# Kernel tuning notes

Measured on AMD Instinct MI355X. Metric: run time of the kernel, lower is better.

The kernel has to match this reference:

```python
import jax, jax.numpy as jnp
import numpy as np

B, T, D = 2, 2048, 2048
HK, HV, K, V = 16, 32, 128, 128          # key heads, value heads, head dims
KEY_DIM, VALUE_DIM = HK * K, HV * V      # 2048, 4096
CONV_W = 4                               # causal conv kernel width
EPS = 1e-6


def setup_inputs() -> dict:
    key = jax.random.key(0)
    ks = jax.random.split(key, 8)
    rn = lambda k, shp, sc: jax.random.normal(k, shp, dtype=jnp.float32) * sc
    return {
        "hidden_states": rn(ks[0], (B, T, D), 1.0),
        "W_qkvz": rn(ks[1], (D, 2 * KEY_DIM + 2 * VALUE_DIM), D ** -0.5),
        "W_ba": rn(ks[2], (D, 2 * HV), D ** -0.5),
        "conv_weight": rn(ks[3], (2 * KEY_DIM + VALUE_DIM, CONV_W), CONV_W ** -0.5),
        "A_log": jnp.log(jax.random.uniform(ks[4], (HV,), minval=1.0, maxval=16.0)),
        "dt_bias": rn(ks[5], (HV,), 0.5),
        "norm_weight": jnp.zeros((V,), jnp.float32),  # zero-centered RMSNorm weight
        "W_out": rn(ks[6], (VALUE_DIM, D), VALUE_DIM ** -0.5),
    }


def _l2norm(x):
    return x * jax.lax.rsqrt(jnp.sum(x * x, axis=-1, keepdims=True) + 1e-6)


def _causal_conv_silu(x, w):
    # x: [B,T,C]; depthwise causal conv, kernel width CONV_W, then SiLU
    xp = jnp.pad(x, ((0, 0), (CONV_W - 1, 0), (0, 0)))
    out = sum(xp[:, j:j + x.shape[1], :] * w[None, None, :, j] for j in range(CONV_W))
    return jax.nn.silu(out)


def _gated_delta_rule(q, k, v, g, beta):
    # q,k: [B,T,HV,K] (l2-normed, q pre-scaled); v: [B,T,HV,V]; g,beta: [B,T,HV]
    def step(S, xs):                      # S: [B,HV,K,V]
        q_t, k_t, v_t, g_t, beta_t = xs
        S = S * jnp.exp(g_t)[..., None, None]
        pred = jnp.einsum('bhk,bhkv->bhv', k_t, S)
        delta = (v_t - pred) * beta_t[..., None]
        S = S + jnp.einsum('bhk,bhv->bhkv', k_t, delta)
        o_t = jnp.einsum('bhk,bhkv->bhv', q_t, S)
        return S, o_t

    mv = lambda x: jnp.moveaxis(x, 1, 0)  # time-major for scan
    S0 = jnp.zeros((q.shape[0], HV, K, V), q.dtype)
    _, o = jax.lax.scan(step, S0, (mv(q), mv(k), mv(v), mv(g), mv(beta)))
    return jnp.moveaxis(o, 0, 1)          # [B,T,HV,V]


def reference(hidden_states, W_qkvz, W_ba, conv_weight, A_log, dt_bias,
              norm_weight, W_out):
    b_, t_ = hidden_states.shape[:2]
    qkvz = hidden_states @ W_qkvz
    q, k, v, z = jnp.split(qkvz, [KEY_DIM, 2 * KEY_DIM, 2 * KEY_DIM + VALUE_DIM], axis=-1)
    ba = hidden_states @ W_ba
    b_gate, a = jnp.split(ba, 2, axis=-1)  # each [B,T,HV]

    # fused causal conv1d + SiLU over concat(q,k,v)
    mixed = _causal_conv_silu(jnp.concatenate([q, k, v], axis=-1), conv_weight)
    q, k, v = jnp.split(mixed, [KEY_DIM, 2 * KEY_DIM], axis=-1)

    # gating: beta = sigmoid(b), g = -exp(A_log) * softplus(a + dt_bias)
    beta = jax.nn.sigmoid(b_gate)
    g = -jnp.exp(A_log) * jax.nn.softplus(a + dt_bias)

    # GQA expand (v_per_k_group = HV // HK), l2norm, scale
    rep = HV // HK
    q = jnp.repeat(q.reshape(b_, t_, HK, K), rep, axis=2)
    k = jnp.repeat(k.reshape(b_, t_, HK, K), rep, axis=2)
    v = v.reshape(b_, t_, HV, V)
    q = _l2norm(q) * (K ** -0.5)
    k = _l2norm(k)

    o = _gated_delta_rule(q, k, v, g, beta)  # [B,T,HV,V]

    # gated RMSNorm (per value head, zero-centered weight) then out projection
    zg = z.reshape(b_, t_, HV, V)
    x = o * jax.nn.silu(zg)
    var = jnp.mean(x * x, axis=-1, keepdims=True)
    x = x * jax.lax.rsqrt(var + EPS) * (1.0 + norm_weight)
    return x.reshape(b_, t_, VALUE_DIM) @ W_out
```

## Files before the change

kernel.cpp:

```cpp
#include <hip/hip_runtime.h>

typedef unsigned short u16;
typedef unsigned int u32;

typedef short bf16x8 __attribute__((ext_vector_type(8)));
typedef float f32x4 __attribute__((ext_vector_type(4)));
typedef float f32x16 __attribute__((ext_vector_type(16)));

#define T_SEQ 2048
#define MFMA16(a, b, c) __builtin_amdgcn_mfma_f32_16x16x32_bf16(a, b, c, 0, 0, 0)
#define MFMA32(a, b, c) __builtin_amdgcn_mfma_f32_32x32x16_bf16(a, b, c, 0, 0, 0)

__device__ __forceinline__ u16 f2bf(float f) {
    u32 u = __float_as_uint(f);
    u += 0x7fffu + ((u >> 16) & 1u);
    return (u16)(u >> 16);
}
__device__ __forceinline__ float bf2f(u16 s) {
    return __uint_as_float(((u32)s) << 16);
}
__device__ __forceinline__ void g2lds16(const u16* gp, u16* lp) {
    __builtin_amdgcn_global_load_lds((const __attribute__((address_space(1))) void*)gp,
                                     (__attribute__((address_space(3))) void*)lp, 16, 0, 0);
}

__global__ __launch_bounds__(256) void cast_f32_bf16(const float* __restrict__ in,
                                                     u16* __restrict__ out, long n) {
    long i = ((long)blockIdx.x * 256 + threadIdx.x) * 4;
    if (i + 3 < n) {
        float4 v = *(const float4*)&in[i];
        out[i + 0] = f2bf(v.x);
        out[i + 1] = f2bf(v.y);
        out[i + 2] = f2bf(v.z);
        out[i + 3] = f2bf(v.w);
    }
}

__global__ __launch_bounds__(256) void transpose_cast(const float* __restrict__ in,
                                                      u16* __restrict__ out, int R, int C) {
    __shared__ float tile[32][33];
    int c0 = blockIdx.x * 32, r0 = blockIdx.y * 32;
    int tx = threadIdx.x & 31, ty = threadIdx.x >> 5;
#pragma unroll
    for (int rr = 0; rr < 32; rr += 8)
        tile[ty + rr][tx] = in[(long)(r0 + ty + rr) * C + c0 + tx];
    __syncthreads();
#pragma unroll
    for (int rr = 0; rr < 32; rr += 8)
        out[(long)(c0 + ty + rr) * R + r0 + tx] = f2bf(tile[tx][ty + rr]);
}

template <int MODE>
__global__ __launch_bounds__(256) void gemm_bt(const u16* __restrict__ A,
                                               const u16* __restrict__ B, void* __restrict__ C,
                                               void* __restrict__ C2, int M, int N, int K, int lda,
                                               int ldb, int ldc) {
    __shared__ __align__(16) u16 As[128 * 64];
    __shared__ __align__(16) u16 Bs[128 * 64];
    int m0 = blockIdx.x * 128, n0 = blockIdx.y * 128;
    int tid = threadIdx.x;
    int lane = tid & 63, w = tid >> 6;
    int wr = w >> 1, wc = w & 1;
    int l31 = lane & 31, hf = lane >> 5;

    f32x16 acc[2][2];
#pragma unroll
    for (int mi = 0; mi < 2; mi++)
#pragma unroll
        for (int nj = 0; nj < 2; nj++)
#pragma unroll
            for (int r = 0; r < 16; r++) acc[mi][nj][r] = 0.f;

    int srow = tid >> 3;
    int sc8 = ((tid & 7) ^ ((tid >> 3) & 7)) * 8;
    const u16* Ag = &A[(long)(m0 + srow) * lda + sc8];
    const u16* Bg = &B[(long)(n0 + srow) * ldb + sc8];

    for (int k0 = 0; k0 < K; k0 += 64) {
#pragma unroll
        for (int p = 0; p < 4; p++) {
            g2lds16(Ag + (long)p * 32 * lda + k0, &As[(p * 256 + tid) * 8]);
            g2lds16(Bg + (long)p * 32 * ldb + k0, &Bs[(p * 256 + tid) * 8]);
        }
        __syncthreads();
#pragma unroll
        for (int ks = 0; ks < 4; ks++) {
            int cell = ((ks * 2 + hf) ^ (l31 & 7)) * 8;
            bf16x8 a0 = *(const bf16x8*)&As[(wr * 64 + l31) * 64 + cell];
            bf16x8 a1 = *(const bf16x8*)&As[(wr * 64 + 32 + l31) * 64 + cell];
            bf16x8 b0 = *(const bf16x8*)&Bs[(wc * 64 + l31) * 64 + cell];
            bf16x8 b1 = *(const bf16x8*)&Bs[(wc * 64 + 32 + l31) * 64 + cell];
            acc[0][0] = MFMA32(a0, b0, acc[0][0]);
            acc[0][1] = MFMA32(a0, b1, acc[0][1]);
            acc[1][0] = MFMA32(a1, b0, acc[1][0]);
            acc[1][1] = MFMA32(a1, b1, acc[1][1]);
        }
        __syncthreads();
    }

    if (MODE == 0) {
#pragma unroll
        for (int mi = 0; mi < 2; mi++)
#pragma unroll
            for (int nj = 0; nj < 2; nj++)
#pragma unroll
                for (int r = 0; r < 16; r++) {
                    int row = m0 + wr * 64 + mi * 32 + (r >> 2) * 8 + hf * 4 + (r & 3);
                    int col = n0 + wc * 64 + nj * 32 + l31;
                    ((float*)C)[(long)row * ldc + col] = acc[mi][nj][r];
                }
    } else {
        u16* dst;
        long dldc;
        int ncol0;
        if (MODE == 2 && n0 >= 8192) {
            dst = (u16*)C2;
            dldc = 4096;
            ncol0 = n0 - 8192;
        } else {
            dst = (u16*)C;
            dldc = (MODE == 2) ? 8192 : ldc;
            ncol0 = n0;
        }
#pragma unroll 1
        for (int half_e = 0; half_e < 2; half_e++) {
            __syncthreads();
            if (wc == half_e) {
#pragma unroll
                for (int mi = 0; mi < 2; mi++)
#pragma unroll
                    for (int nj = 0; nj < 2; nj++)
#pragma unroll
                        for (int r = 0; r < 16; r++) {
                            int row = wr * 64 + mi * 32 + (r >> 2) * 8 + hf * 4 + (r & 3);
                            int col = nj * 32 + l31;
                            u16* base = (row < 64) ? As : Bs;
                            base[(row & 63) * 64 + col] = f2bf(acc[mi][nj][r]);
                        }
            }
            __syncthreads();
#pragma unroll
            for (int rr = 0; rr < 4; rr++) {
                int row = rr * 32 + (tid >> 3), seg = tid & 7;
                u16* base = (row < 64) ? As : Bs;
                *(uint4*)&dst[(long)(m0 + row) * dldc + ncol0 + half_e * 64 + seg * 8] =
                    *(uint4*)&base[(row & 63) * 64 + seg * 8];
            }
        }
    }
}

#define VM8 asm volatile("s_waitcnt vmcnt(8)" ::: "memory")
#define VM4 asm volatile("s_waitcnt vmcnt(4)" ::: "memory")
#define VM0 asm volatile("s_waitcnt vmcnt(0)" ::: "memory")
#define VMNONE ((void)0)

#define STAGE_A(S, R2)                       \
    do {                                     \
        u16* Ld = &sbuf[(R2) * 16384];       \
        long ko = (long)(S) * 32;            \
        g2lds16(pA0 + ko, Ld + dA0);         \
        g2lds16(pA1 + ko, Ld + dA1);         \
    } while (0)
#define STAGE_B(S, R2)                          \
    do {                                        \
        u16* Ld = &sbuf[(R2) * 16384 + 8192];   \
        long ko = (long)(S) * 32;               \
        g2lds16(pB0 + ko, Ld + dA0);            \
        g2lds16(pB1 + ko, Ld + dA1);            \
    } while (0)

#define MQUAD(RB, AV)                          \
    acc[RB][0] = MFMA16(AV, b0, acc[RB][0]);   \
    acc[RB][1] = MFMA16(AV, b1, acc[RB][1]);   \
    acc[RB][2] = MFMA16(AV, b2, acc[RB][2]);   \
    acc[RB][3] = MFMA16(AV, b3, acc[RB][3]);

#define GITER(RING, S3, STG, VMSTMT)                                        \
    {                                                                       \
        const u16* LA = &sbuf[(RING) * 16384 + wm8 * 512 + lane8];          \
        const u16* LB = &sbuf[(RING) * 16384 + 8192 + wn4 * 512 + lane8];   \
        bf16x8 b0 = *(const bf16x8*)&LB[0];                                 \
        bf16x8 b1 = *(const bf16x8*)&LB[512];                               \
        bf16x8 b2 = *(const bf16x8*)&LB[1024];                              \
        bf16x8 b3 = *(const bf16x8*)&LB[1536];                              \
        bf16x8 a0 = *(const bf16x8*)&LA[0];                                 \
        bf16x8 a1 = *(const bf16x8*)&LA[512];                               \
        bf16x8 a2 = *(const bf16x8*)&LA[1024];                              \
        bf16x8 a3 = *(const bf16x8*)&LA[1536];                              \
        bf16x8 a4 = *(const bf16x8*)&LA[2048];                              \
        bf16x8 a5 = *(const bf16x8*)&LA[2560];                              \
        bf16x8 a6 = *(const bf16x8*)&LA[3072];                              \
        bf16x8 a7 = *(const bf16x8*)&LA[3584];                              \
        if (STG) {                                                          \
            STAGE_A(S3, ((RING) + 3) & 3);                                  \
            STAGE_B(S3, ((RING) + 3) & 3);                                  \
        }                                                                   \
        __builtin_amdgcn_s_setprio(1);                                      \
        MQUAD(0, a0)                                                        \
        MQUAD(1, a1)                                                        \
        MQUAD(2, a2)                                                        \
        MQUAD(3, a3)                                                        \
        MQUAD(4, a4)                                                        \
        MQUAD(5, a5)                                                        \
        MQUAD(6, a6)                                                        \
        MQUAD(7, a7)                                                        \
        __builtin_amdgcn_s_setprio(0);                                      \
        VMSTMT;                                                             \
        __builtin_amdgcn_s_barrier();                                       \
        __builtin_amdgcn_sched_barrier(0);                                  \
    }

__global__ __launch_bounds__(512, 2) void gemm256(const u16* __restrict__ A,
                                                  const u16* __restrict__ B,
                                                  u16* __restrict__ Cq, u16* __restrict__ Cz) {
    __shared__ __align__(16) u16 sbuf[65536];
    int bid = blockIdx.x;
    int swz = (bid & 7) * 96 + (bid >> 3);
    int m0 = (swz & 15) * 256;
    int n0 = (swz >> 4) * 256;
    int tid = threadIdx.x;
    int lane = tid & 63, w = tid >> 6;
    int l15 = lane & 15, quad = lane >> 4;
    int wm8 = (w >> 2) * 8, wn4 = (w & 3) * 4;
    int lane8 = lane * 8;
    int dA0 = w * 512 + lane8, dA1 = w * 512 + lane8 + 4096;
    const u16* pA0 = &A[(long)(m0 + w * 16 + l15) * 2048 + quad * 8];
    const u16* pA1 = pA0 + 128L * 2048;
    const u16* pB0 = &B[(long)(n0 + w * 16 + l15) * 2048 + quad * 8];
    const u16* pB1 = pB0 + 128L * 2048;

    f32x4 acc[8][4];
#pragma unroll
    for (int i = 0; i < 8; i++)
#pragma unroll
        for (int j = 0; j < 4; j++) acc[i][j] = (f32x4){0.f, 0.f, 0.f, 0.f};

    STAGE_A(0, 0);
    STAGE_B(0, 0);
    STAGE_A(1, 1);
    STAGE_B(1, 1);
    STAGE_A(2, 2);
    STAGE_B(2, 2);
    VM8;
    __builtin_amdgcn_s_barrier();
    __builtin_amdgcn_sched_barrier(0);

    for (int it = 0; it < 60; it += 4) {
        GITER(0, it + 3, 1, VM8);
        GITER(1, it + 4, 1, VM8);
        GITER(2, it + 5, 1, VM8);
        GITER(3, it + 6, 1, VM8);
    }
    GITER(0, 63, 1, VM8);
    GITER(1, 0, 0, VM4);
    GITER(2, 0, 0, VM0);
    GITER(3, 0, 0, VMNONE);

#pragma unroll
    for (int rb = 0; rb < 8; rb++)
#pragma unroll
        for (int cb = 0; cb < 4; cb++)
#pragma unroll
            for (int r = 0; r < 4; r++) {
                int row = wm8 * 16 + rb * 16 + quad * 4 + r;
                int col = wn4 * 16 + cb * 16 + l15;
                int cg = col >> 4;
                int phys = row * 256 + ((cg ^ (row & 7)) << 4) + (col & 15);
                sbuf[phys] = f2bf(acc[rb][cb][r]);
            }
    __syncthreads();
    u16* dst;
    long dldc;
    int ncol0;
    if (n0 >= 8192) {
        dst = Cz;
        dldc = 4096;
        ncol0 = n0 - 8192;
    } else {
        dst = Cq;
        dldc = 8192;
        ncol0 = n0;
    }
#pragma unroll
    for (int p = 0; p < 16; p++) {
        int row = p * 16 + (tid >> 5);
        int seg = tid & 31;
        int cg = seg >> 1;
        int phys = row * 256 + ((cg ^ (row & 7)) << 4) + (seg & 1) * 8;
        *(uint4*)&dst[(long)(m0 + row) * dldc + ncol0 + seg * 8] = *(const uint4*)&sbuf[phys];
    }
}

__global__ __launch_bounds__(256) void ba_gemm(const u16* __restrict__ hid,
                                               const u16* __restrict__ WbaT,
                                               const float* __restrict__ A_log,
                                               const float* __restrict__ dt_bias,
                                               float* __restrict__ g, float* __restrict__ beta) {
    __shared__ __align__(16) u16 As2[32 * 40];
    __shared__ __align__(16) u16 Bs2[64 * 40];
    int m0 = blockIdx.x * 32;
    int tid = threadIdx.x, lane = tid & 63, w = tid >> 6;
    int quad = lane >> 4, l15 = lane & 15;
    int trow = w & 1;
    int ctile = (w >> 1) * 2;
    f32x4 acc[2];
    acc[0] = (f32x4){0.f, 0.f, 0.f, 0.f};
    acc[1] = (f32x4){0.f, 0.f, 0.f, 0.f};
    int srow = tid >> 2, sc8 = (tid & 3) * 8;
    for (int k0 = 0; k0 < 2048; k0 += 32) {
        if (tid < 128)
            *(uint4*)&As2[srow * 40 + sc8] =
                *(const uint4*)&hid[(long)(m0 + srow) * 2048 + k0 + sc8];
        *(uint4*)&Bs2[srow * 40 + sc8] = *(const uint4*)&WbaT[(long)srow * 2048 + k0 + sc8];
        __syncthreads();
        bf16x8 a = *(const bf16x8*)&As2[(trow * 16 + l15) * 40 + quad * 8];
#pragma unroll
        for (int j = 0; j < 2; j++) {
            bf16x8 b = *(const bf16x8*)&Bs2[((ctile + j) * 16 + l15) * 40 + quad * 8];
            acc[j] = MFMA16(a, b, acc[j]);
        }
        __syncthreads();
    }
#pragma unroll
    for (int j = 0; j < 2; j++)
#pragma unroll
        for (int r = 0; r < 4; r++) {
            int tok = m0 + trow * 16 + quad * 4 + r;
            int col = (ctile + j) * 16 + l15;
            float tot = acc[j][r];
            if (col < 32) {
                beta[(long)tok * 32 + col] = 1.f / (1.f + expf(-tot));
            } else {
                int h = col - 32;
                float x = tot + dt_bias[h];
                float sp = (x > 20.f) ? x : log1pf(expf(x));
                g[(long)tok * 32 + h] = -expf(A_log[h]) * sp;
            }
        }
}

__global__ __launch_bounds__(256) void conv_gate(const u16* __restrict__ qkv,
                                                 const float* __restrict__ conv_w,
                                                 u16* __restrict__ qn, u16* __restrict__ kn,
                                                 u16* __restrict__ vc) {
    int tok = blockIdx.x, tid = threadIdx.x;
    int tloc = tok & (T_SEQ - 1);
    __shared__ float mixed[8192];
    __shared__ float sh_norm[32];
    uint4 zero4;
    zero4.x = zero4.y = zero4.z = zero4.w = 0u;
#pragma unroll
    for (int i = 0; i < 4; i++) {
        int c = (i * 256 + tid) * 8;
        long base = (long)tok * 8192 + c;
        uint4 x3 = *(const uint4*)&qkv[base];
        uint4 x2 = (tloc >= 1) ? *(const uint4*)&qkv[base - 8192] : zero4;
        uint4 x1 = (tloc >= 2) ? *(const uint4*)&qkv[base - 16384] : zero4;
        uint4 x0 = (tloc >= 3) ? *(const uint4*)&qkv[base - 24576] : zero4;
        const u16* p0 = (const u16*)&x0;
        const u16* p1 = (const u16*)&x1;
        const u16* p2 = (const u16*)&x2;
        const u16* p3 = (const u16*)&x3;
#pragma unroll
        for (int e = 0; e < 8; e++) {
            float4 wv = *(const float4*)&conv_w[(long)(c + e) * 4];
            float a = bf2f(p0[e]) * wv.x + bf2f(p1[e]) * wv.y + bf2f(p2[e]) * wv.z +
                      bf2f(p3[e]) * wv.w;
            mixed[c + e] = a / (1.f + __expf(-a));
        }
    }
    __syncthreads();
    int grp = tid >> 3, sub = tid & 7;
    float ss = 0.f;
#pragma unroll
    for (int e = 0; e < 16; e++) {
        float v = mixed[grp * 128 + sub * 16 + e];
        ss += v * v;
    }
    ss += __shfl_xor(ss, 4, 8);
    ss += __shfl_xor(ss, 2, 8);
    ss += __shfl_xor(ss, 1, 8);
    if (sub == 0) sh_norm[grp] = rsqrtf(ss + 1e-6f);
    __syncthreads();
#pragma unroll
    for (int i = 0; i < 4; i++) {
        int c = (i * 256 + tid) * 8;
        float nf = (c < 2048) ? sh_norm[c >> 7] * 0.08838834764831845f
                              : ((c < 4096) ? sh_norm[c >> 7] : 1.f);
        u16 ob[8];
#pragma unroll
        for (int e = 0; e < 8; e++) ob[e] = f2bf(mixed[c + e] * nf);
        uint4 val = *(uint4*)ob;
        if (c < 2048)
            *(uint4*)&qn[(long)tok * 2048 + c] = val;
        else if (c < 4096)
            *(uint4*)&kn[(long)tok * 2048 + (c - 2048)] = val;
        else
            *(uint4*)&vc[(long)tok * 4096 + (c - 4096)] = val;
    }
}

__global__ __launch_bounds__(256) void phaseA(const u16* __restrict__ qn,
                                              const u16* __restrict__ kn,
                                              const u16* __restrict__ vc,
                                              const float* __restrict__ g,
                                              const float* __restrict__ beta,
                                              u16* __restrict__ Tv_g, u16* __restrict__ Tw_g,
                                              u16* __restrict__ Q2_g, u16* __restrict__ obuf) {
    __shared__ __align__(16) u16 kbuf[64][136];
    __shared__ __align__(16) float BMt[64][68];
    __shared__ __align__(16) u16 YT[256][72];
    u16* Lbf = &kbuf[0][0];

    int bid = blockIdx.x;
    int c = bid & 31, h = (bid >> 5) & 31, b = bid >> 10;
    int hk = h >> 1;
    long tokbase = (long)b * T_SEQ + c * 64;
    long cb = (long)bid * 8192;
    int tid = threadIdx.x, lane = tid & 63, w = tid >> 6;
    int quad = lane >> 4, l15 = lane & 15;

    float gl = g[(tokbase + lane) * 32 + h];
    float bl = beta[(tokbase + lane) * 32 + h];
    float cgl = gl;
#pragma unroll
    for (int d = 1; d < 64; d <<= 1) {
        float y = __shfl_up(cgl, d);
        if (lane >= d) cgl += y;
    }
    float wscl = bl * __expf(cgl);
    float eCgl = __expf(cgl);

#pragma unroll
    for (int p = 0; p < 4; p++) {
        int u = p * 256 + tid;
        int row = u >> 4, col8 = (u & 15) * 8;
        *(uint4*)&kbuf[row][col8] = *(const uint4*)&kn[(tokbase + row) * 2048 + hk * 128 + col8];
    }
    __syncthreads();

    {
        f32x4 gk[4];
#pragma unroll
        for (int nj = 0; nj < 4; nj++) gk[nj] = (f32x4){0.f, 0.f, 0.f, 0.f};
#pragma unroll
        for (int kk = 0; kk < 4; kk++) {
            bf16x8 a = *(const bf16x8*)&kbuf[w * 16 + l15][kk * 32 + quad * 8];
#pragma unroll
            for (int nj = 0; nj < 4; nj++) {
                bf16x8 bb = *(const bf16x8*)&kbuf[nj * 16 + l15][kk * 32 + quad * 8];
                gk[nj] = MFMA16(a, bb, gk[nj]);
            }
        }
#pragma unroll
        for (int nj = 0; nj < 4; nj++)
#pragma unroll
            for (int r = 0; r < 4; r++) {
                int i = w * 16 + quad * 4 + r;
                int j = nj * 16 + l15;
                float cgi = __shfl(cgl, i), cgj = __shfl(cgl, j);
                float bi = __shfl(bl, i);
                BMt[j][i] = (j < i) ? bi * gk[nj][r] * __expf(cgi - cgj) : 0.f;
            }
    }
    __syncthreads();

    {
        int col = tid;
        bool isV = col < 128;
        int kcol = col & 127;
        long vbase = tokbase * 4096 + h * 128 + kcol;
        float Yreg[8], acc8[8];
#pragma unroll 1
        for (int bi = 0; bi < 8; ++bi) {
            float vr[8];
            if (isV) {
#pragma unroll
                for (int ii = 0; ii < 8; ii++)
                    vr[ii] = bf2f(vc[vbase + (long)(bi * 8 + ii) * 4096]);
            }
#pragma unroll
            for (int ii = 0; ii < 8; ii++) acc8[ii] = 0.f;
            for (int j = 0; j < bi * 8; ++j) {
                float yv = bf2f(YT[col][j]);
                float4 m0 = *(const float4*)&BMt[j][bi * 8];
                float4 m1 = *(const float4*)&BMt[j][bi * 8 + 4];
                acc8[0] += m0.x * yv;
                acc8[1] += m0.y * yv;
                acc8[2] += m0.z * yv;
                acc8[3] += m0.w * yv;
                acc8[4] += m1.x * yv;
                acc8[5] += m1.y * yv;
                acc8[6] += m1.z * yv;
                acc8[7] += m1.w * yv;
            }
            u16 outb[8];
#pragma unroll
            for (int ii = 0; ii < 8; ii++) {
                int i = bi * 8 + ii;
                float rhs = isV ? __shfl(bl, i) * vr[ii] : __shfl(wscl, i) * bf2f(kbuf[i][kcol]);
                float s = rhs - acc8[ii];
#pragma unroll
                for (int jj = 0; jj < 8; jj++)
                    if (jj < ii) s -= BMt[bi * 8 + jj][i] * Yreg[jj];
                Yreg[ii] = s;
                outb[ii] = f2bf(s);
            }
            *(uint4*)&YT[col][bi * 8] = *(uint4*)outb;
#pragma unroll
            for (int ii = 0; ii < 8; ii++) {
                if (isV)
                    Tv_g[cb + (bi * 8 + ii) * 128 + kcol] = outb[ii];
                else
                    Tw_g[cb + (bi * 8 + ii) * 128 + kcol] = outb[ii];
            }
        }
    }
    __syncthreads();

    {
        f32x4 qk_[4];
#pragma unroll
        for (int nj = 0; nj < 4; nj++) qk_[nj] = (f32x4){0.f, 0.f, 0.f, 0.f};
#pragma unroll
        for (int kk = 0; kk < 4; kk++) {
            bf16x8 a = *(const bf16x8*)&qn[(tokbase + w * 16 + l15) * 2048 + hk * 128 + kk * 32 +
                                           quad * 8];
#pragma unroll
            for (int nj = 0; nj < 4; nj++) {
                bf16x8 bb = *(const bf16x8*)&kbuf[nj * 16 + l15][kk * 32 + quad * 8];
                qk_[nj] = MFMA16(a, bb, qk_[nj]);
            }
        }
        __syncthreads();
#pragma unroll
        for (int nj = 0; nj < 4; nj++)
#pragma unroll
            for (int r = 0; r < 4; r++) {
                int t = w * 16 + quad * 4 + r;
                int rr = nj * 16 + l15;
                float cgt = __shfl(cgl, t), cgr = __shfl(cgl, rr);
                float val = (rr <= t) ? qk_[nj][r] * __expf(cgt - cgr) : 0.f;
                Lbf[t * 72 + rr] = f2bf(val);
            }
    }
    __syncthreads();

#pragma unroll 1
    for (int half = 0; half < 2; half++) {
        f32x4 oa[8];
#pragma unroll
        for (int nj = 0; nj < 8; nj++) oa[nj] = (f32x4){0.f, 0.f, 0.f, 0.f};
#pragma unroll
        for (int kk = 0; kk < 2; kk++) {
            bf16x8 a = *(const bf16x8*)&Lbf[(w * 16 + l15) * 72 + kk * 32 + quad * 8];
#pragma unroll
            for (int nj = 0; nj < 8; nj++) {
                bf16x8 bb = *(const bf16x8*)&YT[half * 128 + nj * 16 + l15][kk * 32 + quad * 8];
                oa[nj] = MFMA16(a, bb, oa[nj]);
            }
        }
        if (half == 0) {
#pragma unroll
            for (int nj = 0; nj < 8; nj++)
#pragma unroll
                for (int r = 0; r < 4; r++) {
                    int t = w * 16 + quad * 4 + r;
                    int vcol = nj * 16 + l15;
                    obuf[(tokbase + t) * 4096 + h * 128 + vcol] = f2bf(oa[nj][r]);
                }
        } else {
#pragma unroll
            for (int nj = 0; nj < 8; nj++)
#pragma unroll
                for (int r = 0; r < 4; r++) {
                    int t = w * 16 + quad * 4 + r;
                    int kcol = nj * 16 + l15;
                    float qsc = __shfl(eCgl, t);
                    float qv = bf2f(qn[(tokbase + t) * 2048 + hk * 128 + kcol]);
                    Q2_g[cb + t * 128 + kcol] = f2bf(qsc * qv - oa[nj][r]);
                }
        }
    }
}

__global__ __launch_bounds__(256) void phaseB(const u16* __restrict__ kn,
                                              const float* __restrict__ g,
                                              const u16* __restrict__ Tv_g,
                                              const u16* __restrict__ Tw_g,
                                              const u16* __restrict__ Q2_g,
                                              u16* __restrict__ obuf) {
    __shared__ __align__(16) float Sf[128][32];
    __shared__ __align__(16) u16 SbfT[32][136];
    __shared__ __align__(16) u16 KhT[128][72];
    __shared__ __align__(16) u16 Ut[32][72];

    int bid = blockIdx.x;
    int vq = bid & 3, h = (bid >> 2) & 31, b = bid >> 7;
    int hk = h >> 1;
    int tid = threadIdx.x, lane = tid & 63, w = tid >> 6;
    int quad = lane >> 4, l15 = lane & 15;

    for (int p = tid; p < 128 * 32; p += 256) ((float*)Sf)[p] = 0.f;
    for (int p = tid; p < 32 * 136; p += 256) ((u16*)SbfT)[p] = 0;
    __syncthreads();

    float gl_pf;
    uint4 kreg[4];
    bf16x8 aTw[4], aQ2[4];
    u16 tvv_pf[2][4], oold[2][4];

#define PB_PREFETCH(cc)                                                                      \
    {                                                                                        \
        long tb_ = (long)b * T_SEQ + (cc) * 64;                                              \
        long cb_ = ((long)((b * 32 + h) * 32) + (cc)) * 8192;                                \
        gl_pf = g[(tb_ + lane) * 32 + h];                                                    \
        const u16* kp_ = &kn[(tb_ + lane) * 2048 + hk * 128 + w * 32];                       \
        kreg[0] = *(const uint4*)&kp_[0];                                                    \
        kreg[1] = *(const uint4*)&kp_[8];                                                    \
        kreg[2] = *(const uint4*)&kp_[16];                                                   \
        kreg[3] = *(const uint4*)&kp_[24];                                                   \
        _Pragma("unroll") for (int kk = 0; kk < 4; kk++) {                                   \
            aTw[kk] = *(const bf16x8*)&Tw_g[cb_ + (w * 16 + l15) * 128 + kk * 32 + quad * 8]; \
            aQ2[kk] = *(const bf16x8*)&Q2_g[cb_ + (w * 16 + l15) * 128 + kk * 32 + quad * 8]; \
        }                                                                                    \
        _Pragma("unroll") for (int nj = 0; nj < 2; nj++) _Pragma("unroll")                   \
            for (int r = 0; r < 4; r++) {                                                    \
            int i_ = w * 16 + quad * 4 + r;                                                  \
            int vg_ = vq * 32 + nj * 16 + l15;                                               \
            tvv_pf[nj][r] = Tv_g[cb_ + (long)i_ * 128 + vg_];                                \
            oold[nj][r] = obuf[(tb_ + i_) * 4096 + h * 128 + vg_];                           \
        }                                                                                    \
    }

    PB_PREFETCH(0);

    for (int c = 0; c < 32; ++c) {
        long tokbase = (long)b * T_SEQ + c * 64;
        float cgl = gl_pf;
#pragma unroll
        for (int d = 1; d < 64; d <<= 1) {
            float y = __shfl_up(cgl, d);
            if (lane >= d) cgl += y;
        }
        float cgC = __shfl(cgl, 63);
        float A_C = __expf(cgC);
        float kscl = __expf(cgC - cgl);

        {
            const u16* kk16 = (const u16*)kreg;
#pragma unroll
            for (int j = 0; j < 32; j++) KhT[w * 32 + j][lane] = f2bf(bf2f(kk16[j]) * kscl);
        }

        f32x4 y1[2], oo[2];
#pragma unroll
        for (int nj = 0; nj < 2; nj++) {
            y1[nj] = (f32x4){0.f, 0.f, 0.f, 0.f};
            oo[nj] = (f32x4){0.f, 0.f, 0.f, 0.f};
        }
#pragma unroll
        for (int kk = 0; kk < 4; kk++) {
#pragma unroll
            for (int nj = 0; nj < 2; nj++) {
                bf16x8 bb = *(const bf16x8*)&SbfT[nj * 16 + l15][kk * 32 + quad * 8];
                y1[nj] = MFMA16(aTw[kk], bb, y1[nj]);
                oo[nj] = MFMA16(aQ2[kk], bb, oo[nj]);
            }
        }
#pragma unroll
        for (int nj = 0; nj < 2; nj++)
#pragma unroll
            for (int r = 0; r < 4; r++) {
                int i = w * 16 + quad * 4 + r;
                int vl = nj * 16 + l15;
                int vg = vq * 32 + vl;
                Ut[vl][i] = f2bf(bf2f(tvv_pf[nj][r]) - y1[nj][r]);
                obuf[(tokbase + i) * 4096 + h * 128 + vg] = f2bf(bf2f(oold[nj][r]) + oo[nj][r]);
            }
        __syncthreads();

        if (c + 1 < 32) PB_PREFETCH(c + 1);

#pragma unroll
        for (int mm = 0; mm < 2; mm++) {
            int mi = 2 * w + mm;
#pragma unroll
            for (int nj = 0; nj < 2; nj++) {
                f32x4 sacc;
#pragma unroll
                for (int r = 0; r < 4; r++)
                    sacc[r] = A_C * Sf[mi * 16 + quad * 4 + r][nj * 16 + l15];
#pragma unroll
                for (int kk = 0; kk < 2; kk++) {
                    bf16x8 a = *(const bf16x8*)&KhT[mi * 16 + l15][kk * 32 + quad * 8];
                    bf16x8 bb = *(const bf16x8*)&Ut[nj * 16 + l15][kk * 32 + quad * 8];
                    sacc = MFMA16(a, bb, sacc);
                }
#pragma unroll
                for (int r = 0; r < 4; r++) {
                    int kd = mi * 16 + quad * 4 + r, vl = nj * 16 + l15;
                    Sf[kd][vl] = sacc[r];
                    SbfT[vl][kd] = f2bf(sacc[r]);
                }
            }
        }
        __syncthreads();
    }
#undef PB_PREFETCH
}

__global__ __launch_bounds__(256) void gated_norm(const u16* __restrict__ obuf,
                                                  const u16* __restrict__ zbuf,
                                                  const float* __restrict__ norm_w,
                                                  u16* __restrict__ xn) {
    int tok = blockIdx.x, tid = threadIdx.x;
    long obase = (long)tok * 4096 + tid * 16;
    u16 ob[16], zb[16];
    *(uint4*)(ob + 0) = *(const uint4*)&obuf[obase];
    *(uint4*)(ob + 8) = *(const uint4*)&obuf[obase + 8];
    *(uint4*)(zb + 0) = *(const uint4*)&zbuf[obase];
    *(uint4*)(zb + 8) = *(const uint4*)&zbuf[obase + 8];
    float x[16];
    float ss = 0.f;
#pragma unroll
    for (int i = 0; i < 16; i++) {
        float ov = bf2f(ob[i]);
        float zv = bf2f(zb[i]);
        float xv = ov * (zv / (1.f + expf(-zv)));
        x[i] = xv;
        ss += xv * xv;
    }
    ss += __shfl_xor(ss, 4, 8);
    ss += __shfl_xor(ss, 2, 8);
    ss += __shfl_xor(ss, 1, 8);
    float scale = rsqrtf(ss * (1.f / 128.f) + 1e-6f);
    int cbase = (tid * 16) & 127;
#pragma unroll
    for (int i = 0; i < 16; i++)
        xn[(long)tok * 4096 + tid * 16 + i] = f2bf(x[i] * scale * (1.f + norm_w[cbase + i]));
}

extern "C" void kernel_launch(void* const* d_in, const int* in_sizes, int n_in, void* d_out,
                              int out_size, void* d_ws, size_t ws_size, hipStream_t stream) {
    const float* hidden = (const float*)d_in[0];
    const float* W_qkvz = (const float*)d_in[1];
    const float* W_ba = (const float*)d_in[2];
    const float* conv_w = (const float*)d_in[3];
    const float* A_log = (const float*)d_in[4];
    const float* dt_bias = (const float*)d_in[5];
    const float* norm_w = (const float*)d_in[6];
    const float* W_out = (const float*)d_in[7];
    float* out = (float*)d_out;

    char* ws = (char*)d_ws;
    u16* wqT = (u16*)(ws + 0);
    u16* qn = (u16*)(ws + 0);
    u16* vc = (u16*)(ws + 16777216L);
    u16* hidbf = (u16*)(ws + 50331648L);
    u16* kn = (u16*)(ws + 50331648L);
    u16* woT = (u16*)(ws + 67108864L);
    u16* qkv_raw = (u16*)(ws + 83886080L);
    u16* Tv = (u16*)(ws + 83886080L);
    u16* Tw = (u16*)(ws + 117440512L);
    u16* xn = (u16*)(ws + 83886080L);
    u16* WbaT = (u16*)(ws + 150994944L);
    u16* zbuf = (u16*)(ws + 150994944L);
    u16* Q2 = (u16*)(ws + 184549376L);
    float* g = (float*)(ws + 218103808L);
    float* beta = (float*)(ws + 218628096L);
    u16* obuf = vc;

    cast_f32_bf16<<<8192, 256, 0, stream>>>(hidden, hidbf, 8388608L);
    transpose_cast<<<dim3(384, 64), 256, 0, stream>>>(W_qkvz, wqT, 2048, 12288);
    transpose_cast<<<dim3(64, 128), 256, 0, stream>>>(W_out, woT, 4096, 2048);
    transpose_cast<<<dim3(2, 64), 256, 0, stream>>>(W_ba, WbaT, 2048, 64);
    ba_gemm<<<128, 256, 0, stream>>>(hidbf, WbaT, A_log, dt_bias, g, beta);
    gemm256<<<768, 512, 0, stream>>>(hidbf, wqT, qkv_raw, zbuf);
    conv_gate<<<4096, 256, 0, stream>>>(qkv_raw, conv_w, qn, kn, vc);
    phaseA<<<2048, 256, 0, stream>>>(qn, kn, vc, g, beta, Tv, Tw, Q2, obuf);
    phaseB<<<256, 256, 0, stream>>>(kn, g, Tv, Tw, Q2, obuf);
    gated_norm<<<4096, 256, 0, stream>>>(obuf, zbuf, norm_w, xn);
    gemm_bt<0><<<dim3(32, 16), 256, 0, stream>>>(xn, woT, out, nullptr, 4096, 2048, 4096, 4096,
                                                 4096, 2048);
}
```

Before: 935.5 us.

## Stage GEMM tiles through registers instead of direct global-to-LDS loads

Replaces the direct global_load_lds staging in the 256x256 GEMM main loop with register-staged prefetch. Each stage is loaded into VGPRs two iterations ahead and written to the LDS ring one iteration later. Explicit vmcnt waits are dropped in favor of an lgkmcnt(0) wait before each barrier. This trades the hardware direct-to-LDS path for more register pressure (16 extra uint4 per thread at 2 waves/SIMD) and lets the compiler insert waits on the global loads, which may stall MFMA issue.

```diff
diff --git a/kernel.cpp b/kernel.cpp
--- a/kernel.cpp
+++ b/kernel.cpp
@@ -150,24 +150,22 @@
     }
 }
 
-#define VM8 asm volatile("s_waitcnt vmcnt(8)" ::: "memory")
-#define VM4 asm volatile("s_waitcnt vmcnt(4)" ::: "memory")
-#define VM0 asm volatile("s_waitcnt vmcnt(0)" ::: "memory")
-#define VMNONE ((void)0)
-
-#define STAGE_A(S, R2)                       \
-    do {                                     \
-        u16* Ld = &sbuf[(R2) * 16384];       \
-        long ko = (long)(S) * 32;            \
-        g2lds16(pA0 + ko, Ld + dA0);         \
-        g2lds16(pA1 + ko, Ld + dA1);         \
+
+#define ISSUE4(S, T)                                   \
+    do {                                               \
+        long ko = (long)(S) * 32;                      \
+        gA0[T] = *(const uint4*)(pA0 + ko);            \
+        gA1[T] = *(const uint4*)(pA1 + ko);            \
+        gB0[T] = *(const uint4*)(pB0 + ko);            \
+        gB1[T] = *(const uint4*)(pB1 + ko);            \
     } while (0)
-#define STAGE_B(S, R2)                          \
-    do {                                        \
-        u16* Ld = &sbuf[(R2) * 16384 + 8192];   \
-        long ko = (long)(S) * 32;               \
-        g2lds16(pB0 + ko, Ld + dA0);            \
-        g2lds16(pB1 + ko, Ld + dA1);            \
+#define WRITE4(R2, T)                                  \
+    do {                                               \
+        u16* Ld = &sbuf[(R2) * 16384];                 \
+        *(uint4*)&Ld[dA0] = gA0[T];                    \
+        *(uint4*)&Ld[dA1] = gA1[T];                    \
+        *(uint4*)&Ld[8192 + dA0] = gB0[T];             \
+        *(uint4*)&Ld[8192 + dA1] = gB1[T];             \
     } while (0)
 
 #define MQUAD(RB, AV)                          \
@@ -176,7 +174,7 @@
     acc[RB][2] = MFMA16(AV, b2, acc[RB][2]);   \
     acc[RB][3] = MFMA16(AV, b3, acc[RB][3]);
 
-#define GITER(RING, S3, STG, VMSTMT)                                        \
+#define GITER(RING, SNXT, ISET, DOI, WRING, WSET, DOW)                      \
     {                                                                       \
         const u16* LA = &sbuf[(RING) * 16384 + wm8 * 512 + lane8];          \
         const u16* LB = &sbuf[(RING) * 16384 + 8192 + wn4 * 512 + lane8];   \
@@ -192,10 +190,8 @@
         bf16x8 a5 = *(const bf16x8*)&LA[2560];                              \
         bf16x8 a6 = *(const bf16x8*)&LA[3072];                              \
         bf16x8 a7 = *(const bf16x8*)&LA[3584];                              \
-        if (STG) {                                                          \
-            STAGE_A(S3, ((RING) + 3) & 3);                                  \
-            STAGE_B(S3, ((RING) + 3) & 3);                                  \
-        }                                                                   \
+        if (DOI) ISSUE4(SNXT, ISET);                                        \
+        if (DOW) WRITE4(WRING, WSET);                                       \
         __builtin_amdgcn_s_setprio(1);                                      \
         MQUAD(0, a0)                                                        \
         MQUAD(1, a1)                                                        \
@@ -206,7 +202,7 @@
         MQUAD(6, a6)                                                        \
         MQUAD(7, a7)                                                        \
         __builtin_amdgcn_s_setprio(0);                                      \
-        VMSTMT;                                                             \
+        asm volatile("s_waitcnt lgkmcnt(0)" ::: "memory");                  \
         __builtin_amdgcn_s_barrier();                                       \
         __builtin_amdgcn_sched_barrier(0);                                  \
     }
@@ -230,32 +226,31 @@
     const u16* pB0 = &B[(long)(n0 + w * 16 + l15) * 2048 + quad * 8];
     const u16* pB1 = pB0 + 128L * 2048;
 
+    uint4 gA0[2], gA1[2], gB0[2], gB1[2];
+
     f32x4 acc[8][4];
 #pragma unroll
     for (int i = 0; i < 8; i++)
 #pragma unroll
         for (int j = 0; j < 4; j++) acc[i][j] = (f32x4){0.f, 0.f, 0.f, 0.f};
 
-    STAGE_A(0, 0);
-    STAGE_B(0, 0);
-    STAGE_A(1, 1);
-    STAGE_B(1, 1);
-    STAGE_A(2, 2);
-    STAGE_B(2, 2);
-    VM8;
+    ISSUE4(0, 0);
+    ISSUE4(1, 1);
+    WRITE4(0, 0);
+    asm volatile("s_waitcnt lgkmcnt(0)" ::: "memory");
     __builtin_amdgcn_s_barrier();
     __builtin_amdgcn_sched_barrier(0);
 
     for (int it = 0; it < 60; it += 4) {
-        GITER(0, it + 3, 1, VM8);
-        GITER(1, it + 4, 1, VM8);
-        GITER(2, it + 5, 1, VM8);
-        GITER(3, it + 6, 1, VM8);
-    }
-    GITER(0, 63, 1, VM8);
-    GITER(1, 0, 0, VM4);
-    GITER(2, 0, 0, VM0);
-    GITER(3, 0, 0, VMNONE);
+        GITER(0, it + 2, 0, 1, 1, 1, 1);
+        GITER(1, it + 3, 1, 1, 2, 0, 1);
+        GITER(2, it + 4, 0, 1, 3, 1, 1);
+        GITER(3, it + 5, 1, 1, 0, 0, 1);
+    }
+    GITER(0, 62, 0, 1, 1, 1, 1);
+    GITER(1, 63, 1, 1, 2, 0, 1);
+    GITER(2, 0, 0, 0, 3, 1, 1);
+    GITER(3, 0, 0, 0, 0, 0, 0);
 
 #pragma unroll
     for (int rb = 0; rb < 8; rb++)
```

Measured after the change: 1.152 ms. 23.1% more time.

## Split phaseB state across 8 value slices to double block count

Applied to the files above, without the earlier changes.

The sequential chunk-recurrence kernel now splits the 128-wide value dimension into 8 slices of 16 instead of 4 slices of 32, launching 512 blocks instead of 256. On a GPU with 256 CUs, this is meant to occupy more of the machine during the serial-over-chunks phase and to shorten each block's per-chunk critical path. The cost is that each block redundantly reloads and rescales the K, Tw and Q2 tiles, which doubles that traffic and the KhT construction work.

```diff
diff --git a/kernel.cpp b/kernel.cpp
--- a/kernel.cpp
+++ b/kernel.cpp
@@ -591,25 +591,25 @@
                                               const u16* __restrict__ Tw_g,
                                               const u16* __restrict__ Q2_g,
                                               u16* __restrict__ obuf) {
-    __shared__ __align__(16) float Sf[128][32];
-    __shared__ __align__(16) u16 SbfT[32][136];
+    __shared__ __align__(16) float Sf[128][16];
+    __shared__ __align__(16) u16 SbfT[16][136];
     __shared__ __align__(16) u16 KhT[128][72];
-    __shared__ __align__(16) u16 Ut[32][72];
+    __shared__ __align__(16) u16 Ut[16][72];
 
     int bid = blockIdx.x;
-    int vq = bid & 3, h = (bid >> 2) & 31, b = bid >> 7;
+    int vq = bid & 7, h = (bid >> 3) & 31, b = bid >> 8;
     int hk = h >> 1;
     int tid = threadIdx.x, lane = tid & 63, w = tid >> 6;
     int quad = lane >> 4, l15 = lane & 15;
 
-    for (int p = tid; p < 128 * 32; p += 256) ((float*)Sf)[p] = 0.f;
-    for (int p = tid; p < 32 * 136; p += 256) ((u16*)SbfT)[p] = 0;
+    for (int p = tid; p < 128 * 16; p += 256) ((float*)Sf)[p] = 0.f;
+    for (int p = tid; p < 16 * 136; p += 256) ((u16*)SbfT)[p] = 0;
     __syncthreads();
 
     float gl_pf;
     uint4 kreg[4];
     bf16x8 aTw[4], aQ2[4];
-    u16 tvv_pf[2][4], oold[2][4];
+    u16 tvv_pf[4], oold[4];
 
 #define PB_PREFETCH(cc)                                                                      \
     {                                                                                        \
@@ -625,12 +625,11 @@
             aTw[kk] = *(const bf16x8*)&Tw_g[cb_ + (w * 16 + l15) * 128 + kk * 32 + quad * 8]; \
             aQ2[kk] = *(const bf16x8*)&Q2_g[cb_ + (w * 16 + l15) * 128 + kk * 32 + quad * 8]; \
         }                                                                                    \
-        _Pragma("unroll") for (int nj = 0; nj < 2; nj++) _Pragma("unroll")                   \
-            for (int r = 0; r < 4; r++) {                                                    \
+        _Pragma("unroll") for (int r = 0; r < 4; r++) {                                      \
             int i_ = w * 16 + quad * 4 + r;                                                  \
-            int vg_ = vq * 32 + nj * 16 + l15;                                               \
-            tvv_pf[nj][r] = Tv_g[cb_ + (long)i_ * 128 + vg_];                                \
-            oold[nj][r] = obuf[(tb_ + i_) * 4096 + h * 128 + vg_];                           \
+            int vg_ = vq * 16 + l15;                                                         \
+            tvv_pf[r] = Tv_g[cb_ + (long)i_ * 128 + vg_];                                    \
+            oold[r] = obuf[(tb_ + i_) * 4096 + h * 128 + vg_];                               \
         }                                                                                    \
     }
 
@@ -654,31 +653,21 @@
             for (int j = 0; j < 32; j++) KhT[w * 32 + j][lane] = f2bf(bf2f(kk16[j]) * kscl);
         }
 
-        f32x4 y1[2], oo[2];
-#pragma unroll
-        for (int nj = 0; nj < 2; nj++) {
-            y1[nj] = (f32x4){0.f, 0.f, 0.f, 0.f};
-            oo[nj] = (f32x4){0.f, 0.f, 0.f, 0.f};
-        }
+        f32x4 y1 = (f32x4){0.f, 0.f, 0.f, 0.f};
+        f32x4 oo = (f32x4){0.f, 0.f, 0.f, 0.f};
 #pragma unroll
         for (int kk = 0; kk < 4; kk++) {
-#pragma unroll
-            for (int nj = 0; nj < 2; nj++) {
-                bf16x8 bb = *(const bf16x8*)&SbfT[nj * 16 + l15][kk * 32 + quad * 8];
-                y1[nj] = MFMA16(aTw[kk], bb, y1[nj]);
-                oo[nj] = MFMA16(aQ2[kk], bb, oo[nj]);
-            }
-        }
-#pragma unroll
-        for (int nj = 0; nj < 2; nj++)
-#pragma unroll
-            for (int r = 0; r < 4; r++) {
-                int i = w * 16 + quad * 4 + r;
-                int vl = nj * 16 + l15;
-                int vg = vq * 32 + vl;
-                Ut[vl][i] = f2bf(bf2f(tvv_pf[nj][r]) - y1[nj][r]);
-                obuf[(tokbase + i) * 4096 + h * 128 + vg] = f2bf(bf2f(oold[nj][r]) + oo[nj][r]);
-            }
+            bf16x8 bb = *(const bf16x8*)&SbfT[l15][kk * 32 + quad * 8];
+            y1 = MFMA16(aTw[kk], bb, y1);
+            oo = MFMA16(aQ2[kk], bb, oo);
+        }
+#pragma unroll
+        for (int r = 0; r < 4; r++) {
+            int i = w * 16 + quad * 4 + r;
+            int vg = vq * 16 + l15;
+            Ut[l15][i] = f2bf(bf2f(tvv_pf[r]) - y1[r]);
+            obuf[(tokbase + i) * 4096 + h * 128 + vg] = f2bf(bf2f(oold[r]) + oo[r]);
+        }
         __syncthreads();
 
         if (c + 1 < 32) PB_PREFETCH(c + 1);
@@ -686,24 +675,21 @@
 #pragma unroll
         for (int mm = 0; mm < 2; mm++) {
             int mi = 2 * w + mm;
-#pragma unroll
-            for (int nj = 0; nj < 2; nj++) {
-                f32x4 sacc;
-#pragma unroll
-                for (int r = 0; r < 4; r++)
-                    sacc[r] = A_C * Sf[mi * 16 + quad * 4 + r][nj * 16 + l15];
-#pragma unroll
-                for (int kk = 0; kk < 2; kk++) {
-                    bf16x8 a = *(const bf16x8*)&KhT[mi * 16 + l15][kk * 32 + quad * 8];
-                    bf16x8 bb = *(const bf16x8*)&Ut[nj * 16 + l15][kk * 32 + quad * 8];
-                    sacc = MFMA16(a, bb, sacc);
-                }
-#pragma unroll
-                for (int r = 0; r < 4; r++) {
-                    int kd = mi * 16 + quad * 4 + r, vl = nj * 16 + l15;
-                    Sf[kd][vl] = sacc[r];
-                    SbfT[vl][kd] = f2bf(sacc[r]);
-                }
+            f32x4 sacc;
+#pragma unroll
+            for (int r = 0; r < 4; r++)
+                sacc[r] = A_C * Sf[mi * 16 + quad * 4 + r][l15];
+#pragma unroll
+            for (int kk = 0; kk < 2; kk++) {
+                bf16x8 a = *(const bf16x8*)&KhT[mi * 16 + l15][kk * 32 + quad * 8];
+                bf16x8 bb = *(const bf16x8*)&Ut[l15][kk * 32 + quad * 8];
+                sacc = MFMA16(a, bb, sacc);
+            }
+#pragma unroll
+            for (int r = 0; r < 4; r++) {
+                int kd = mi * 16 + quad * 4 + r;
+                Sf[kd][l15] = sacc[r];
+                SbfT[l15][kd] = f2bf(sacc[r]);
             }
         }
         __syncthreads();
@@ -780,7 +766,7 @@
     gemm256<<<768, 512, 0, stream>>>(hidbf, wqT, qkv_raw, zbuf);
     conv_gate<<<4096, 256, 0, stream>>>(qkv_raw, conv_w, qn, kn, vc);
     phaseA<<<2048, 256, 0, stream>>>(qn, kn, vc, g, beta, Tv, Tw, Q2, obuf);
-    phaseB<<<256, 256, 0, stream>>>(kn, g, Tv, Tw, Q2, obuf);
+    phaseB<<<512, 256, 0, stream>>>(kn, g, Tv, Tw, Q2, obuf);
     gated_norm<<<4096, 256, 0, stream>>>(obuf, zbuf, norm_w, xn);
     gemm_bt<0><<<dim3(32, 16), 256, 0, stream>>>(xn, woT, out, nullptr, 4096, 2048, 4096, 4096,
                                                  4096, 2048);
```

After: 995.2 us. +6.4%, slower.
